# Kernel tuning notes

Hardware: AMD Instinct MI355X
Metric: run time of the kernel (lower is better)

The kernel has to match this reference:

```python
import jax, jax.numpy as jnp
import numpy as np

EPS = 1e-06

def elu_feature_map(x):
    return jax.nn.elu(x) + 1.0

def setup_inputs() -> dict:
    key = jax.random.key(0)
    kq, kk, kv = jax.random.split(key, 3)
    shape = (4, 8, 4096, 64)  # [B, H, L, D]
    return {
        "queries": jax.random.normal(kq, shape, dtype=jnp.float32),
        "keys": jax.random.normal(kk, shape, dtype=jnp.float32),
        "values": jax.random.normal(kv, shape, dtype=jnp.float32),
    }

def reference(queries, keys, values):
    Q = elu_feature_map(queries)            # [b,h,l,d]
    K = elu_feature_map(keys)               # [b,h,l,d]
    v_length = values.shape[-2]
    values_n = values / v_length            # [b,h,l,v]
    KV = jnp.einsum('bhld,bhlv->bhdv', K, values_n)          # [b,h,d,v]
    Z = 1.0 / (jnp.einsum('bhld,bhd->bhl', Q, K.sum(axis=-2)) + EPS)  # [b,h,l]
    out = jnp.einsum('bhld,bhdv,bhl->bhlv', Q, KV, Z) * v_length
    return out
```

## Files before the change

kernel.cpp:

```cpp
#include <hip/hip_runtime.h>


#define LSEQ   4096
#define DDIM   64
#define NHEAD  32
#define CHUNKS 32
#define ROWSB  (LSEQ / CHUNKS)
#define TILE   16
#define WSPH   (DDIM * DDIM + DDIM)

__device__ __forceinline__ float fmap(float x) {
    return x > 0.0f ? (x + 1.0f) : __expf(x);
}

__device__ __forceinline__ void fma4(float4& a, float s, const float4& b) {
    a.x = fmaf(s, b.x, a.x);
    a.y = fmaf(s, b.y, a.y);
    a.z = fmaf(s, b.z, a.z);
    a.w = fmaf(s, b.w, a.w);
}

__global__ __launch_bounds__(256) void la_kv_kernel(
    const float* __restrict__ Kg, const float* __restrict__ Vg,
    float* __restrict__ ws)
{
    __shared__ float klds[TILE * DDIM];
    __shared__ float vlds[TILE * DDIM];
    __shared__ float red[WSPH];

    const int t    = threadIdx.x;
    const int wave = t >> 6;
    const int lane = t & 63;
    const int dq   = lane >> 3;
    const int vq   = lane & 7;

    const int bh    = blockIdx.x / CHUNKS;
    const int chunk = blockIdx.x % CHUNKS;
    const size_t base = (size_t)bh * LSEQ * DDIM + (size_t)chunk * ROWSB * DDIM;
    const float* Kb = Kg + base;
    const float* Vb = Vg + base;
    const float invL = 1.0f / (float)LSEQ;

    float acc[8][8];
    float ksum[8];
#pragma unroll
    for (int i = 0; i < 8; ++i) {
        ksum[i] = 0.0f;
#pragma unroll
        for (int j = 0; j < 8; ++j) acc[i][j] = 0.0f;
    }

    for (int tile = 0; tile < ROWSB / TILE; ++tile) {
        __syncthreads();
        float4 kx = ((const float4*)(Kb + tile * TILE * DDIM))[t];
        kx.x = fmap(kx.x); kx.y = fmap(kx.y); kx.z = fmap(kx.z); kx.w = fmap(kx.w);
        ((float4*)klds)[t] = kx;
        float4 vx = ((const float4*)(Vb + tile * TILE * DDIM))[t];
        vx.x *= invL; vx.y *= invL; vx.z *= invL; vx.w *= invL;
        ((float4*)vlds)[t] = vx;
        __syncthreads();

#pragma unroll
        for (int r = 0; r < 4; ++r) {
            const int l = wave * 4 + r;
            const float4 ka = *(const float4*)(klds + l * DDIM + dq * 8);
            const float4 kb = *(const float4*)(klds + l * DDIM + dq * 8 + 4);
            const float4 va = *(const float4*)(vlds + l * DDIM + vq * 4);
            const float4 vb = *(const float4*)(vlds + l * DDIM + 32 + vq * 4);
            const float kk[8] = {ka.x, ka.y, ka.z, ka.w, kb.x, kb.y, kb.z, kb.w};
            const float vv[8] = {va.x, va.y, va.z, va.w, vb.x, vb.y, vb.z, vb.w};
#pragma unroll
            for (int i = 0; i < 8; ++i) {
                ksum[i] += kk[i];
#pragma unroll
                for (int j = 0; j < 8; ++j)
                    acc[i][j] = fmaf(kk[i], vv[j], acc[i][j]);
            }
        }
    }

    for (int w = 0; w < 4; ++w) {
        __syncthreads();
        if (wave == w) {
#pragma unroll
            for (int i = 0; i < 8; ++i) {
                const int d = dq * 8 + i;
                float* p = red + d * DDIM + vq * 4;
                float4 lo = make_float4(acc[i][0], acc[i][1], acc[i][2], acc[i][3]);
                float4 hi = make_float4(acc[i][4], acc[i][5], acc[i][6], acc[i][7]);
                if (w != 0) {
                    const float4 plo = *(const float4*)p;
                    const float4 phi = *(const float4*)(p + 32);
                    lo.x += plo.x; lo.y += plo.y; lo.z += plo.z; lo.w += plo.w;
                    hi.x += phi.x; hi.y += phi.y; hi.z += phi.z; hi.w += phi.w;
                }
                *(float4*)p = lo;
                *(float4*)(p + 32) = hi;
            }
            if (vq == 0) {
                float* p = red + DDIM * DDIM + dq * 8;
                float4 s0 = make_float4(ksum[0], ksum[1], ksum[2], ksum[3]);
                float4 s1 = make_float4(ksum[4], ksum[5], ksum[6], ksum[7]);
                if (w != 0) {
                    const float4 p0 = *(const float4*)p;
                    const float4 p1 = *(const float4*)(p + 4);
                    s0.x += p0.x; s0.y += p0.y; s0.z += p0.z; s0.w += p0.w;
                    s1.x += p1.x; s1.y += p1.y; s1.z += p1.z; s1.w += p1.w;
                }
                *(float4*)p = s0;
                *(float4*)(p + 4) = s1;
            }
        }
    }
    __syncthreads();

    float* dst = ws + (size_t)bh * WSPH;
    for (int i = t; i < WSPH; i += 256)
        unsafeAtomicAdd(dst + i, red[i]);
}

#define QSTRIDE 68

__global__ __launch_bounds__(256) void la_out_kernel(
    const float* __restrict__ Qg, const float* __restrict__ ws,
    float* __restrict__ out)
{
    __shared__ float kvlds[DDIM * DDIM];
    __shared__ float ksl[DDIM];
    __shared__ float qlds[128 * QSTRIDE];
    __shared__ float zs[128];

    const int t    = threadIdx.x;
    const int bh   = blockIdx.x >> 5;
    const int tile = blockIdx.x & 31;
    const size_t base = (size_t)bh * LSEQ * DDIM + (size_t)tile * 128 * DDIM;
    const float* Qb = Qg + base;
    float* Ob = out + base;

    const float4* wsrc = (const float4*)(ws + (size_t)bh * WSPH);
    for (int i = t; i < 1040; i += 256) {
        const float4 x = wsrc[i];
        if (i < 1024) ((float4*)kvlds)[i] = x;
        else          ((float4*)ksl)[i - 1024] = x;
    }

#pragma unroll
    for (int i = 0; i < 8; ++i) {
        const int o = t + i * 256;
        float4 q = ((const float4*)Qb)[o];
        q.x = fmap(q.x); q.y = fmap(q.y); q.z = fmap(q.z); q.w = fmap(q.w);
        const int row = o >> 4;
        const int c4  = o & 15;
        *(float4*)(qlds + row * QSTRIDE + c4 * 4) = q;
    }
    __syncthreads();

    {
        const int row  = t >> 1;
        const int half = t & 1;
        float s = 0.0f;
#pragma unroll
        for (int i = 0; i < 8; ++i) {
            const float4 q  = *(const float4*)(qlds + row * QSTRIDE + half * 32 + i * 4);
            const float4 ks = *(const float4*)(ksl + half * 32 + i * 4);
            s += q.x * ks.x + q.y * ks.y + q.z * ks.z + q.w * ks.w;
        }
        s += __shfl_xor(s, 1);
        if (half == 0) zs[row] = (float)LSEQ / (s + 1e-6f);
    }
    __syncthreads();

    const int vq = t & 7;
    const int rg = t >> 3;
    float4 accL[4], accH[4];
#pragma unroll
    for (int r = 0; r < 4; ++r) {
        accL[r] = make_float4(0.f, 0.f, 0.f, 0.f);
        accH[r] = make_float4(0.f, 0.f, 0.f, 0.f);
    }

    for (int d4 = 0; d4 < 16; ++d4) {
        float4 kvlo[4], kvhi[4];
#pragma unroll
        for (int i = 0; i < 4; ++i) {
            kvlo[i] = *(const float4*)(kvlds + (d4 * 4 + i) * DDIM + vq * 4);
            kvhi[i] = *(const float4*)(kvlds + (d4 * 4 + i) * DDIM + 32 + vq * 4);
        }
#pragma unroll
        for (int r = 0; r < 4; ++r) {
            const float4 q = *(const float4*)(qlds + (rg * 4 + r) * QSTRIDE + d4 * 4);
            fma4(accL[r], q.x, kvlo[0]);
            fma4(accL[r], q.y, kvlo[1]);
            fma4(accL[r], q.z, kvlo[2]);
            fma4(accL[r], q.w, kvlo[3]);
            fma4(accH[r], q.x, kvhi[0]);
            fma4(accH[r], q.y, kvhi[1]);
            fma4(accH[r], q.z, kvhi[2]);
            fma4(accH[r], q.w, kvhi[3]);
        }
    }

#pragma unroll
    for (int r = 0; r < 4; ++r) {
        const int row = rg * 4 + r;
        const float z = zs[row];
        float4 o = accL[r];
        o.x *= z; o.y *= z; o.z *= z; o.w *= z;
        *(float4*)(Ob + row * DDIM + vq * 4) = o;
        o = accH[r];
        o.x *= z; o.y *= z; o.z *= z; o.w *= z;
        *(float4*)(Ob + row * DDIM + 32 + vq * 4) = o;
    }
}

extern "C" void kernel_launch(void* const* d_in, const int* in_sizes, int n_in,
                              void* d_out, int out_size, void* d_ws, size_t ws_size,
                              hipStream_t stream) {
    const float* q = (const float*)d_in[0];
    const float* k = (const float*)d_in[1];
    const float* v = (const float*)d_in[2];
    float* o  = (float*)d_out;
    float* ws = (float*)d_ws;

    hipMemsetAsync(d_ws, 0, (size_t)NHEAD * WSPH * sizeof(float), stream);
    hipLaunchKernelGGL(la_kv_kernel, dim3(NHEAD * CHUNKS), dim3(256), 0, stream,
                       k, v, ws);
    hipLaunchKernelGGL(la_out_kernel, dim3(NHEAD * (LSEQ / 128)), dim3(256), 0, stream,
                       q, ws, o);
}
```

Baseline: 62.32 us.

## Replace atomic KV accumulation with per-chunk partials and a separate reduce kernel

Each KV block now writes its partial KV and ksum tile to its own workspace slot with plain float4 stores instead of atomically adding into a shared per-head buffer. A new reduce kernel sums the 32 chunk partials per head, and the memset is dropped. This removes atomic contention and the memset launch, at the cost of an extra kernel launch and more workspace traffic, about 17MB written and read back.

```diff
diff --git a/kernel.cpp b/kernel.cpp
--- a/kernel.cpp
+++ b/kernel.cpp
@@ -8,6 +8,7 @@
 #define ROWSB  (LSEQ / CHUNKS)
 #define TILE   16
 #define WSPH   (DDIM * DDIM + DDIM)
+#define WSPH4  (WSPH / 4)
 
 __device__ __forceinline__ float fmap(float x) {
     return x > 0.0f ? (x + 1.0f) : __expf(x);
@@ -114,15 +115,35 @@
     }
     __syncthreads();
 
-    float* dst = ws + (size_t)bh * WSPH;
-    for (int i = t; i < WSPH; i += 256)
-        unsafeAtomicAdd(dst + i, red[i]);
+    float4* dst = (float4*)(ws + (size_t)blockIdx.x * WSPH);
+    const float4* src = (const float4*)red;
+    for (int i = t; i < WSPH4; i += 256)
+        dst[i] = src[i];
+}
+
+__global__ __launch_bounds__(256) void la_reduce_kernel(
+    const float* __restrict__ ws, float* __restrict__ kvout)
+{
+    const int h   = blockIdx.x / 5;
+    const int seg = blockIdx.x % 5;
+    const int t   = threadIdx.x;
+    if (t >= 208) return;
+    const int i4 = seg * 208 + t;
+
+    const float4* base = (const float4*)(ws + (size_t)h * CHUNKS * WSPH) + i4;
+    float4 acc = make_float4(0.f, 0.f, 0.f, 0.f);
+#pragma unroll 8
+    for (int p = 0; p < CHUNKS; ++p) {
+        const float4 x = base[(size_t)p * WSPH4];
+        acc.x += x.x; acc.y += x.y; acc.z += x.z; acc.w += x.w;
+    }
+    ((float4*)(kvout + (size_t)h * WSPH))[i4] = acc;
 }
 
 #define QSTRIDE 68
 
 __global__ __launch_bounds__(256) void la_out_kernel(
-    const float* __restrict__ Qg, const float* __restrict__ ws,
+    const float* __restrict__ Qg, const float* __restrict__ kvin,
     float* __restrict__ out)
 {
     __shared__ float kvlds[DDIM * DDIM];
@@ -137,7 +158,7 @@
     const float* Qb = Qg + base;
     float* Ob = out + base;
 
-    const float4* wsrc = (const float4*)(ws + (size_t)bh * WSPH);
+    const float4* wsrc = (const float4*)(kvin + (size_t)bh * WSPH);
     for (int i = t; i < 1040; i += 256) {
         const float4 x = wsrc[i];
         if (i < 1024) ((float4*)kvlds)[i] = x;
@@ -221,10 +242,12 @@
     const float* v = (const float*)d_in[2];
     float* o  = (float*)d_out;
     float* ws = (float*)d_ws;
-
-    hipMemsetAsync(d_ws, 0, (size_t)NHEAD * WSPH * sizeof(float), stream);
+    float* kvfinal = ws + (size_t)NHEAD * CHUNKS * WSPH;
+
     hipLaunchKernelGGL(la_kv_kernel, dim3(NHEAD * CHUNKS), dim3(256), 0, stream,
                        k, v, ws);
+    hipLaunchKernelGGL(la_reduce_kernel, dim3(NHEAD * 5), dim3(256), 0, stream,
+                       ws, kvfinal);
     hipLaunchKernelGGL(la_out_kernel, dim3(NHEAD * (LSEQ / 128)), dim3(256), 0, stream,
-                       q, ws, o);
-}
+                       q, kvfinal, o);
+}
```

Result: faster. 57.14 us (-8.3%).
